# Optimization experiments

Hardware: AMD Instinct MI355X
Metric: run time of the kernel (lower is better)

## Reference

```python
import jax, jax.numpy as jnp
import numpy as np

N = 20000      # nodes (spots)
D = 256        # embed_dim
H = 4          # n_heads
DH = D // H    # head dim
L = 2          # n_layers
E = 320000     # edges (avg degree 16)
K = 48         # static padded-neighbor cap (>= true max degree for this data)
EPS = 1e-5
NEG = -1e30


def setup_inputs() -> dict:
    key = jax.random.key(0)
    ks = jax.random.split(key, 8)
    s = 0.05
    return {
        "expr_embed": jax.random.normal(ks[0], (N, D), jnp.float32),
        "spatial_embed": jax.random.normal(ks[1], (N, D), jnp.float32),
        "in_proj_w": jax.random.normal(ks[2], (L, 3 * D, D), jnp.float32) * s,
        "in_proj_b": jnp.zeros((L, 3 * D), jnp.float32),
        "out_proj_w": jax.random.normal(ks[3], (L, D, D), jnp.float32) * s,
        "out_proj_b": jnp.zeros((L, D), jnp.float32),
        "ffn_w1": jax.random.normal(ks[4], (L, 2 * D, D), jnp.float32) * s,
        "ffn_b1": jnp.zeros((L, 2 * D), jnp.float32),
        "ffn_w2": jax.random.normal(ks[5], (L, D, 2 * D), jnp.float32) * s,
        "ffn_b2": jnp.zeros((L, D), jnp.float32),
        "ln1_g": jnp.ones((L, D), jnp.float32),
        "ln1_b": jnp.zeros((L, D), jnp.float32),
        "ln2_g": jnp.ones((L, D), jnp.float32),
        "ln2_b": jnp.zeros((L, D), jnp.float32),
        "edge_index": jax.random.randint(ks[6], (2, E), 0, N, jnp.int32),
    }


def _build_neighbors(edge_index):
    """Padded neighbor indices (N,K) and key_padding_mask (N,K) (True = pad)."""
    src, tgt = edge_index[0], edge_index[1]
    counts = jnp.zeros((N,), jnp.int32).at[tgt].add(1)
    order = jnp.argsort(tgt)                       # group edges by target
    src_s, tgt_s = src[order], tgt[order]
    offsets = jnp.concatenate([jnp.zeros((1,), jnp.int32),
                               jnp.cumsum(counts)[:-1].astype(jnp.int32)])
    pos = jnp.arange(E, dtype=jnp.int32) - offsets[tgt_s]
    pos = jnp.where(pos < K, pos, K)               # K is out-of-bounds -> dropped
    nbr = jnp.zeros((N, K), jnp.int32).at[tgt_s, pos].set(src_s, mode='drop')
    pad = jnp.ones((N, K), bool).at[tgt_s, pos].set(False, mode='drop')
    iso = counts == 0                              # isolated spots attend to self
    nbr = nbr.at[:, 0].set(jnp.where(iso, jnp.arange(N, dtype=jnp.int32), nbr[:, 0]))
    pad = pad.at[:, 0].set(jnp.where(iso, False, pad[:, 0]))
    return nbr, pad


def _layernorm(x, g, b):
    mu = jnp.mean(x, -1, keepdims=True)
    var = jnp.var(x, -1, keepdims=True)
    return (x - mu) * jax.lax.rsqrt(var + EPS) * g + b


def _forward(expr_embed, spatial_embed, in_proj_w, in_proj_b, out_proj_w,
             out_proj_b, ffn_w1, ffn_b1, ffn_w2, ffn_b2,
             ln1_g, ln1_b, ln2_g, ln2_b, nbr, pad):
    x = expr_embed
    scale = 1.0 / jnp.sqrt(jnp.asarray(DH, x.dtype))
    for i in range(L):
        Wq, Wk, Wv = jnp.split(in_proj_w[i], 3, axis=0)
        bq, bk, bv = jnp.split(in_proj_b[i], 3, axis=0)
        q = (x @ Wq.T + bq).reshape(N, H, DH)
        # project spatial once, gather projected rows (same math as gather-then-project)
        k = (spatial_embed @ Wk.T + bk)[nbr].reshape(N, K, H, DH)
        v = (spatial_embed @ Wv.T + bv)[nbr].reshape(N, K, H, DH)
        scores = jnp.einsum('nhd,nkhd->nhk', q, k) * scale      # (N,H,K)
        scores = jnp.where(pad[:, None, :], NEG, scores)
        attn = jax.nn.softmax(scores, axis=-1)
        ao = jnp.einsum('nhk,nkhd->nhd', attn, v).reshape(N, D)
        ao = ao @ out_proj_w[i].T + out_proj_b[i]
        x = _layernorm(x + ao, ln1_g[i], ln1_b[i])
        h = jax.nn.gelu(x @ ffn_w1[i].T + ffn_b1[i], approximate=False)
        h = h @ ffn_w2[i].T + ffn_b2[i]
        x = _layernorm(x + h, ln2_g[i], ln2_b[i])
    return x


def reference(expr_embed, spatial_embed, in_proj_w, in_proj_b, out_proj_w,
              out_proj_b, ffn_w1, ffn_b1, ffn_w2, ffn_b2,
              ln1_g, ln1_b, ln2_g, ln2_b, edge_index):
    nbr, pad = _build_neighbors(edge_index.astype(jnp.int32))
    return _forward(expr_embed, spatial_embed, in_proj_w, in_proj_b, out_proj_w,
                    out_proj_b, ffn_w1, ffn_b1, ffn_w2, ffn_b2,
                    ln1_g, ln1_b, ln2_g, ln2_b, nbr, pad)
```

## Files before the change

kernel.cpp:

```cpp
#include <hip/hip_runtime.h>

#define N_NODES 20000
#define DIM 256
#define NHEAD 4
#define DHEAD 64
#define NLAYER 2
#define NEDGE 320000
#define KCAP 48
#define NBM64 313
#define NBM32 625

typedef __bf16 v8bf __attribute__((ext_vector_type(8)));
typedef __bf16 v2bf __attribute__((ext_vector_type(2)));
typedef float v4f __attribute__((ext_vector_type(4)));

union U32 { unsigned u; v2bf v; };

__device__ __forceinline__ unsigned short f2bf(float f) {
    unsigned u = __float_as_uint(f);
    unsigned r = u + 0x7FFFu + ((u >> 16) & 1u);
    return (unsigned short)(r >> 16);
}
__device__ __forceinline__ float bflo(unsigned u) { return __uint_as_float(u << 16); }
__device__ __forceinline__ float bfhi(unsigned u) { return __uint_as_float(u & 0xFFFF0000u); }

__device__ __forceinline__ void gl2lds(const void* g, void* l) {
    __builtin_amdgcn_global_load_lds(
        (const __attribute__((address_space(1))) unsigned int*)g,
        (__attribute__((address_space(3))) unsigned int*)l, 16, 0, 0);
}

__device__ __forceinline__ void stage8(const unsigned short* __restrict__ g0,
                                       size_t stride_e, unsigned short* lds) {
    const int l = threadIdx.x & 63;
    const int r = l >> 3;
    const int c = (l & 7) ^ r;
    gl2lds(g0 + (size_t)r * stride_e + c * 8, lds);
}
__device__ __forceinline__ void stage8c(const unsigned short* __restrict__ base,
                                        int row0, int rowmax, size_t stride_e,
                                        int k0, unsigned short* lds) {
    const int l = threadIdx.x & 63;
    const int r = l >> 3;
    const int c = (l & 7) ^ r;
    int row = row0 + r; row = row > rowmax ? rowmax : row;
    gl2lds(base + (size_t)row * stride_e + k0 + c * 8, lds);
}

__device__ __forceinline__ v8bf frag_read(const unsigned short* lds, int row, int col2) {
    const int bo = row * 128 + (col2 ^ ((row & 7) << 4));
    return *(const v8bf*)((const char*)lds + bo);
}

__global__ void sniffzero_kernel(const unsigned short* __restrict__ p,
                                 int* __restrict__ flag, int* __restrict__ cnt) {
    if (blockIdx.x == 0) {
        __shared__ int s;
        if (threadIdx.x == 0) s = 0;
        __syncthreads();
        int c = 0;
        for (int i = threadIdx.x; i < 4096; i += 256) {
            unsigned short u = p[i];
            unsigned e = (u >> 7) & 0xFFu;
            if (e == 0xFFu) c++;
            else if (e == 0u && (u & 0x7Fu)) c++;
        }
        atomicAdd(&s, c);
        __syncthreads();
        if (threadIdx.x == 0) flag[0] = (s >= 4) ? 1 : 0;
    } else {
        int i = (blockIdx.x - 1) * 256 + threadIdx.x;
        if (i < N_NODES) cnt[i] = 0;
    }
}

struct ConvBfArgs { const void* src[6]; unsigned short* dst[6]; int n[6]; };
struct ConvF32Args { const void* src[8]; float* dst[8]; int n[8]; };

__global__ void prep_kernel(ConvBfArgs a, ConvF32Args cf,
                            const int* __restrict__ ei,
                            int* __restrict__ cnt, int* __restrict__ nbr,
                            const int* __restrict__ flag) {
    const int y = blockIdx.y;
    if (y < 6) {
        const int n  = a.n[y];
        const int i0 = (blockIdx.x * 256 + threadIdx.x) * 4;
        if (i0 >= n) return;
        unsigned short* dst = a.dst[y];
        if (flag[0]) {
            float4 v = *(const float4*)((const float*)a.src[y] + i0);
            ushort4 o;
            o.x = f2bf(v.x); o.y = f2bf(v.y); o.z = f2bf(v.z); o.w = f2bf(v.w);
            *(ushort4*)(dst + i0) = o;
        } else {
            ushort4 u = *(const ushort4*)((const unsigned short*)a.src[y] + i0);
            *(ushort4*)(dst + i0) = u;
        }
    } else if (y == 6) {
        if (blockIdx.x >= 2) return;
        const int i0 = (blockIdx.x * 256 + threadIdx.x) * 4;
        const int f = flag[0];
#pragma unroll
        for (int t = 0; t < 8; ++t) {
            const int n = cf.n[t];
            if (i0 >= n) continue;
            float* dst = cf.dst[t];
            if (f) {
                float4 v = *(const float4*)((const float*)cf.src[t] + i0);
                *(float4*)(dst + i0) = v;
            } else {
                ushort4 u = *(const ushort4*)((const unsigned short*)cf.src[t] + i0);
                *(float4*)(dst + i0) =
                    make_float4(bflo(u.x), bflo(u.y), bflo(u.z), bflo(u.w));
            }
        }
    } else {
        const int e = blockIdx.x * 256 + threadIdx.x;
        if (e >= NEDGE) return;
        int s = ei[e];
        int t = ei[NEDGE + e];
        int slot = atomicAdd(&cnt[t], 1);
        if (slot < KCAP) nbr[t * KCAP + slot] = s;
    }
}

__device__ __forceinline__ void gemm_body64(
    unsigned short* At, unsigned short* Bt,
    const unsigned short* __restrict__ A, const unsigned short* __restrict__ B,
    const float* __restrict__ bias, unsigned short* __restrict__ C,
    int M, int Nc, int Kd, int m0, int nB, int nC, int do_gelu)
{
    const int tid  = threadIdx.x;
    const int wave = tid >> 6;
    const int lane = tid & 63;
    const int wr   = (wave >> 1) * 32;
    const int wc   = (wave & 1) * 64;
    const int lm   = lane & 15;
    const int lk   = (lane >> 4) * 8;

    v4f acc[2][4] = {};

    for (int k0 = 0; k0 < Kd; k0 += 64) {
#pragma unroll
        for (int i = 0; i < 2; ++i) {
            const int rr = wave * 16 + i * 8;
            stage8c(A, m0 + rr, M - 1, Kd, k0, At + rr * 64);
        }
#pragma unroll
        for (int i = 0; i < 4; ++i) {
            const int rr = wave * 32 + i * 8;
            stage8(B + (size_t)(nB + rr) * Kd + k0, Kd, Bt + rr * 64);
        }
        __syncthreads();

#pragma unroll
        for (int ks = 0; ks < 2; ++ks) {
            v8bf af[2], bq[4];
#pragma unroll
            for (int mi = 0; mi < 2; ++mi)
                af[mi] = frag_read(At, wr + mi * 16 + lm, (ks * 32 + lk) * 2);
#pragma unroll
            for (int ni = 0; ni < 4; ++ni)
                bq[ni] = frag_read(Bt, wc + ni * 16 + lm, (ks * 32 + lk) * 2);
#pragma unroll
            for (int mi = 0; mi < 2; ++mi)
#pragma unroll
                for (int ni = 0; ni < 4; ++ni)
                    acc[mi][ni] = __builtin_amdgcn_mfma_f32_16x16x32_bf16(
                        af[mi], bq[ni], acc[mi][ni], 0, 0, 0);
        }
        __syncthreads();
    }

    const int rq = (lane >> 4) << 2;
#pragma unroll
    for (int ni = 0; ni < 4; ++ni) {
        int colb = wc + ni * 16 + lm;
        float bv = bias[nB + colb];
        int colc = nC + colb;
#pragma unroll
        for (int mi = 0; mi < 2; ++mi) {
#pragma unroll
            for (int r = 0; r < 4; ++r) {
                int row = m0 + wr + mi * 16 + rq + r;
                if (row >= M) continue;
                float v = acc[mi][ni][r] + bv;
                if (do_gelu) v = 0.5f * v * (1.0f + erff(v * 0.7071067811865475f));
                C[(size_t)row * Nc + colc] = f2bf(v);
            }
        }
    }
}

__global__ __launch_bounds__(256) void gemm_kernel(
    const unsigned short* __restrict__ A, const unsigned short* __restrict__ B,
    const float* __restrict__ bias, unsigned short* __restrict__ C,
    int M, int Nc, int Kd, int do_gelu)
{
    __shared__ __align__(1024) unsigned short At[64 * 64];
    __shared__ __align__(1024) unsigned short Bt[128 * 64];
    const int n0 = blockIdx.y * 128;
    gemm_body64(At, Bt, A, B, bias, C, M, Nc, Kd, blockIdx.x * 64, n0, n0, do_gelu);
}

__global__ __launch_bounds__(256) void qkv_kernel(
    const unsigned short* __restrict__ x, const unsigned short* __restrict__ spat,
    const unsigned short* __restrict__ W, const float* __restrict__ bias,
    unsigned short* __restrict__ q, unsigned short* __restrict__ kv, int M)
{
    __shared__ __align__(1024) unsigned short At[64 * 64];
    __shared__ __align__(1024) unsigned short Bt[128 * 64];
    const int y = blockIdx.y;
    const unsigned short* A = (y < 2) ? x : spat;
    unsigned short*       C = (y < 2) ? q : kv;
    const int Nc = (y < 2) ? 256 : 512;
    const int nB = y * 128;
    const int nC = (y < 2) ? nB : nB - 256;
    gemm_body64(At, Bt, A, W, bias, C, M, Nc, 256, blockIdx.x * 64, nB, nC, 0);
}

__global__ __launch_bounds__(256) void gemm_ln_kernel(
    const unsigned short* __restrict__ A, const unsigned short* __restrict__ B,
    const float* __restrict__ bias, const unsigned short* __restrict__ xres,
    const float* __restrict__ g, const float* __restrict__ bb,
    unsigned short* __restrict__ xout, void* __restrict__ dout,
    int M, int Kd, int final_out, const int* __restrict__ flag)
{
    __shared__ __align__(1024) unsigned short At[32 * 64];
    __shared__ __align__(1024) unsigned short Bt[256 * 64];
    __shared__ float partS[4][32], partSS[4][32];
    __shared__ float totMu[32], totR[32];

    const int tid  = threadIdx.x;
    const int m0   = blockIdx.x * 32;
    const int wave = tid >> 6;
    const int lane = tid & 63;
    const int wn0  = wave * 64;
    const int lm   = lane & 15;
    const int lk   = (lane >> 4) * 8;

    v4f acc[2][4] = {};

    for (int k0 = 0; k0 < Kd; k0 += 64) {
        {
            const int rr = wave * 8;
            stage8c(A, m0 + rr, M - 1, Kd, k0, At + rr * 64);
        }
#pragma unroll
        for (int i = 0; i < 8; ++i) {
            const int rr = wave * 64 + i * 8;
            stage8(B + (size_t)rr * Kd + k0, Kd, Bt + rr * 64);
        }
        __syncthreads();

#pragma unroll
        for (int ks = 0; ks < 2; ++ks) {
            v8bf af[2], bq[4];
#pragma unroll
            for (int mi = 0; mi < 2; ++mi)
                af[mi] = frag_read(At, mi * 16 + lm, (ks * 32 + lk) * 2);
#pragma unroll
            for (int ni = 0; ni < 4; ++ni)
                bq[ni] = frag_read(Bt, wn0 + ni * 16 + lm, (ks * 32 + lk) * 2);
#pragma unroll
            for (int mi = 0; mi < 2; ++mi)
#pragma unroll
                for (int ni = 0; ni < 4; ++ni)
                    acc[mi][ni] = __builtin_amdgcn_mfma_f32_16x16x32_bf16(
                        af[mi], bq[ni], acc[mi][ni], 0, 0, 0);
        }
        __syncthreads();
    }

    const int rq = (lane >> 4) << 2;
    float gv[4], bv2[4], biasv[4];
#pragma unroll
    for (int ni = 0; ni < 4; ++ni) {
        int col = wn0 + ni * 16 + lm;
        biasv[ni] = bias[col];
        gv[ni]    = g[col];
        bv2[ni]   = bb[col];
    }

    float sl[2][4] = {}, ssl[2][4] = {};
#pragma unroll
    for (int mi = 0; mi < 2; ++mi) {
#pragma unroll
        for (int r = 0; r < 4; ++r) {
            int row = m0 + mi * 16 + rq + r;
#pragma unroll
            for (int ni = 0; ni < 4; ++ni) {
                int col = wn0 + ni * 16 + lm;
                float resv = bflo((unsigned)xres[(size_t)row * DIM + col]);
                float v = acc[mi][ni][r] + biasv[ni] + resv;
                acc[mi][ni][r] = v;
                sl[mi][r]  += v;
                ssl[mi][r] += v * v;
            }
        }
    }
#pragma unroll
    for (int mi = 0; mi < 2; ++mi)
#pragma unroll
        for (int r = 0; r < 4; ++r) {
#pragma unroll
            for (int m = 1; m <= 8; m <<= 1) {
                sl[mi][r]  += __shfl_xor(sl[mi][r],  m, 64);
                ssl[mi][r] += __shfl_xor(ssl[mi][r], m, 64);
            }
        }
    if (lm == 0) {
#pragma unroll
        for (int mi = 0; mi < 2; ++mi)
#pragma unroll
            for (int r = 0; r < 4; ++r) {
                partS[wave][mi * 16 + rq + r]  = sl[mi][r];
                partSS[wave][mi * 16 + rq + r] = ssl[mi][r];
            }
    }
    __syncthreads();
    if (tid < 32) {
        float S = partS[0][tid] + partS[1][tid] + partS[2][tid] + partS[3][tid];
        float SS = partSS[0][tid] + partSS[1][tid] + partSS[2][tid] + partSS[3][tid];
        float mu  = S * (1.0f / DIM);
        float var = SS * (1.0f / DIM) - mu * mu;
        totMu[tid] = mu;
        totR[tid]  = rsqrtf(var + 1e-5f);
    }
    __syncthreads();

#pragma unroll
    for (int mi = 0; mi < 2; ++mi) {
#pragma unroll
        for (int r = 0; r < 4; ++r) {
            int lrow = mi * 16 + rq + r;
            int row  = m0 + lrow;
            float mu = totMu[lrow];
            float rv = totR[lrow];
#pragma unroll
            for (int ni = 0; ni < 4; ++ni) {
                int col = wn0 + ni * 16 + lm;
                float o = (acc[mi][ni][r] - mu) * rv * gv[ni] + bv2[ni];
                if (final_out) {
                    if (flag[0]) ((float*)dout)[(size_t)row * DIM + col] = o;
                    else ((unsigned short*)dout)[(size_t)row * DIM + col] = f2bf(o);
                } else {
                    xout[(size_t)row * DIM + col] = f2bf(o);
                }
            }
        }
    }
}

__global__ __launch_bounds__(256) void attn_kernel(
    const unsigned short* __restrict__ q,
    const unsigned short* __restrict__ kv,
    const int* __restrict__ nbr,
    const int* __restrict__ cnt,
    unsigned short* __restrict__ ao)
{
    const int n    = blockIdx.x;
    const int tid  = threadIdx.x;
    const int h    = tid >> 6;
    const int lane = tid & 63;

    __shared__ float sc[NHEAD][KCAP];
    __shared__ int   nbs[NHEAD][KCAP];

    int deg = cnt[n];
    if (deg > KCAP) deg = KCAP;
    const bool iso = (deg == 0);
    if (iso) deg = 1;

    if (lane < KCAP)
        nbs[h][lane] = (lane < deg) ? (iso ? n : nbr[n * KCAP + lane]) : 0;

    const int sub = lane & 7;
    const int grp = lane >> 3;
    const uint4 qu = *(const uint4*)&q[(size_t)n * DIM + h * DHEAD + sub * 8];
    const unsigned short* kbase = kv + h * DHEAD + sub * 8;
    const int nit = (deg + 7) >> 3;

    const int quarter = lane >> 4;
    const int d0      = (lane & 15) * 4;
    const unsigned short* vbase = kv + 256 + h * DHEAD + d0;
    const int dmax = (deg + 3) & ~3;
    const int npv  = dmax >> 2;

    uint4 ku[6];
#pragma unroll
    for (int it = 0; it < 6; ++it) {
        if (it < nit) {
            int nb = nbs[h][it * 8 + grp];
            ku[it] = *(const uint4*)&kbase[(size_t)nb * 512];
        }
    }
    uint2 vu[8];
#pragma unroll
    for (int it = 0; it < 8; ++it) {
        if (it < npv) {
            int nb = nbs[h][it * 4 + quarter];
            vu[it] = *(const uint2*)&vbase[(size_t)nb * 512];
        }
    }

#pragma unroll
    for (int it = 0; it < 6; ++it) {
        if (it < nit) {
            int j = it * 8 + grp;
            uint4 kz = ku[it];
#if __has_builtin(__builtin_amdgcn_fdot2_f32_bf16)
            U32 a0{qu.x}, a1{qu.y}, a2{qu.z}, a3{qu.w};
            U32 b0{kz.x}, b1{kz.y}, b2{kz.z}, b3{kz.w};
            float p = __builtin_amdgcn_fdot2_f32_bf16(a0.v, b0.v, 0.0f, false);
            p = __builtin_amdgcn_fdot2_f32_bf16(a1.v, b1.v, p, false);
            p = __builtin_amdgcn_fdot2_f32_bf16(a2.v, b2.v, p, false);
            p = __builtin_amdgcn_fdot2_f32_bf16(a3.v, b3.v, p, false);
#else
            float p = bflo(qu.x) * bflo(kz.x);
            p = fmaf(bfhi(qu.x), bfhi(kz.x), p);
            p = fmaf(bflo(qu.y), bflo(kz.y), p);
            p = fmaf(bfhi(qu.y), bfhi(kz.y), p);
            p = fmaf(bflo(qu.z), bflo(kz.z), p);
            p = fmaf(bfhi(qu.z), bfhi(kz.z), p);
            p = fmaf(bflo(qu.w), bflo(kz.w), p);
            p = fmaf(bfhi(qu.w), bfhi(kz.w), p);
#endif
            p += __shfl_xor(p, 1, 64);
            p += __shfl_xor(p, 2, 64);
            p += __shfl_xor(p, 4, 64);
            if (sub == 0 && j < deg) sc[h][j] = p * 0.125f;
        }
    }

    {
        float s  = (lane < deg) ? sc[h][lane] : -1e30f;
        float mx = s;
#pragma unroll
        for (int m = 32; m >= 1; m >>= 1) mx = fmaxf(mx, __shfl_xor(mx, m, 64));
        float e   = (lane < deg) ? __expf(s - mx) : 0.0f;
        float sum = e;
#pragma unroll
        for (int m = 32; m >= 1; m >>= 1) sum += __shfl_xor(sum, m, 64);
        float inv = 1.0f / sum;
        if (lane < KCAP) sc[h][lane] = e * inv;
    }

    {
        float a0 = 0.f, a1 = 0.f, a2 = 0.f, a3 = 0.f;
#pragma unroll
        for (int it = 0; it < 8; ++it) {
            if (it < npv) {
                float w = sc[h][it * 4 + quarter];
                uint2 u = vu[it];
                a0 = fmaf(w, bflo(u.x), a0);
                a1 = fmaf(w, bfhi(u.x), a1);
                a2 = fmaf(w, bflo(u.y), a2);
                a3 = fmaf(w, bfhi(u.y), a3);
            }
        }
        for (int j = 32; j < dmax; j += 4) {
            int j0 = j + quarter;
            int nb = nbs[h][j0];
            uint2 u = *(const uint2*)&vbase[(size_t)nb * 512];
            float w = sc[h][j0];
            a0 = fmaf(w, bflo(u.x), a0);
            a1 = fmaf(w, bfhi(u.x), a1);
            a2 = fmaf(w, bflo(u.y), a2);
            a3 = fmaf(w, bfhi(u.y), a3);
        }
        a0 += __shfl_xor(a0, 16, 64); a0 += __shfl_xor(a0, 32, 64);
        a1 += __shfl_xor(a1, 16, 64); a1 += __shfl_xor(a1, 32, 64);
        a2 += __shfl_xor(a2, 16, 64); a2 += __shfl_xor(a2, 32, 64);
        a3 += __shfl_xor(a3, 16, 64); a3 += __shfl_xor(a3, 32, 64);
        if (lane < 16) {
            uint2 o;
            o.x = (unsigned)f2bf(a0) | ((unsigned)f2bf(a1) << 16);
            o.y = (unsigned)f2bf(a2) | ((unsigned)f2bf(a3) << 16);
            *(uint2*)&ao[(size_t)n * DIM + h * DHEAD + d0] = o;
        }
    }
}

extern "C" void kernel_launch(void* const* d_in, const int* in_sizes, int n_in,
                              void* d_out, int out_size, void* d_ws, size_t ws_size,
                              hipStream_t stream) {
    const int* ei = (const int*)d_in[14];

    char* ws = (char*)d_ws;
    size_t off = 0;
    auto alloc = [&](size_t bytes) -> void* {
        void* p = ws + off;
        off = (off + bytes + 255) & ~(size_t)255;
        return p;
    };

    const int bidx[6] = { 0, 1, 2, 4, 6, 8 };
    const int bnn[6]  = { N_NODES * DIM, N_NODES * DIM,
                          NLAYER * 3 * DIM * DIM, NLAYER * DIM * DIM,
                          NLAYER * 2 * DIM * DIM, NLAYER * DIM * 2 * DIM };
    ConvBfArgs cb;
    unsigned short* canb[6];
    for (int i = 0; i < 6; ++i) {
        canb[i] = (unsigned short*)alloc((size_t)bnn[i] * 2);
        cb.src[i] = d_in[bidx[i]];
        cb.dst[i] = canb[i];
        cb.n[i]   = bnn[i];
    }
    const unsigned short* expr_b = canb[0];
    const unsigned short* spat_b = canb[1];
    const unsigned short* ipw    = canb[2];
    const unsigned short* opw    = canb[3];
    const unsigned short* w1     = canb[4];
    const unsigned short* w2     = canb[5];

    const int fidx[8] = { 3, 5, 7, 9, 10, 11, 12, 13 };
    const int fn[8]   = { NLAYER * 3 * DIM, NLAYER * DIM, NLAYER * 2 * DIM,
                          NLAYER * DIM, NLAYER * DIM, NLAYER * DIM,
                          NLAYER * DIM, NLAYER * DIM };
    ConvF32Args cf;
    float* canf[8];
    for (int i = 0; i < 8; ++i) {
        canf[i] = (float*)alloc((size_t)fn[i] * 4);
        cf.src[i] = d_in[fidx[i]];
        cf.dst[i] = canf[i];
        cf.n[i]   = fn[i];
    }

    unsigned short* x_buf  = (unsigned short*)alloc((size_t)N_NODES * DIM * 2);
    unsigned short* q_buf  = (unsigned short*)alloc((size_t)N_NODES * DIM * 2);
    unsigned short* kv_buf = (unsigned short*)alloc((size_t)N_NODES * 2 * DIM * 2);
    unsigned short* ao_buf = (unsigned short*)alloc((size_t)N_NODES * DIM * 2);
    unsigned short* h_buf  = (unsigned short*)alloc((size_t)N_NODES * 2 * DIM * 2);
    int* cnt  = (int*)alloc((size_t)N_NODES * 4);
    int* nbr  = (int*)alloc((size_t)N_NODES * KCAP * 4);
    int* flag = (int*)alloc(256);

    sniffzero_kernel<<<1 + (N_NODES + 255) / 256, 256, 0, stream>>>(
        (const unsigned short*)d_in[0], flag, cnt);
    prep_kernel<<<dim3((N_NODES * DIM) / 1024, 8), 256, 0, stream>>>(
        cb, cf, ei, cnt, nbr, flag);

    for (int i = 0; i < NLAYER; ++i) {
        const unsigned short* Wqkv = ipw + (size_t)i * 3 * DIM * DIM;
        const float*          bqkv = canf[0] + (size_t)i * 3 * DIM;
        const unsigned short* xin  = (i == 0) ? expr_b : x_buf;

        qkv_kernel<<<dim3(NBM64, 6), 256, 0, stream>>>(
            xin, spat_b, Wqkv, bqkv, q_buf, kv_buf, N_NODES);
        attn_kernel<<<N_NODES, 256, 0, stream>>>(q_buf, kv_buf, nbr, cnt, ao_buf);
        gemm_ln_kernel<<<NBM32, 256, 0, stream>>>(
            ao_buf, opw + (size_t)i * DIM * DIM, canf[1] + (size_t)i * DIM,
            xin, canf[4] + (size_t)i * DIM, canf[5] + (size_t)i * DIM,
            x_buf, nullptr, N_NODES, DIM, 0, flag);
        gemm_kernel<<<dim3(NBM64, 4), 256, 0, stream>>>(
            x_buf, w1 + (size_t)i * 2 * DIM * DIM, canf[2] + (size_t)i * 2 * DIM,
            h_buf, N_NODES, 2 * DIM, DIM, 1);
        gemm_ln_kernel<<<NBM32, 256, 0, stream>>>(
            h_buf, w2 + (size_t)i * DIM * 2 * DIM, canf[3] + (size_t)i * DIM,
            x_buf, canf[6] + (size_t)i * DIM, canf[7] + (size_t)i * DIM,
            x_buf, d_out, N_NODES, 2 * DIM, (i == NLAYER - 1) ? 1 : 0, flag);
    }
}
```

Before: 398.3 us.

## Replace LDS-staged GEMM tiles with direct global-to-register double-buffered fragment loads

GEMM and GEMM+LayerNorm kernels stop staging A/B tiles through shared memory with global_load_lds and barriers. Each wave now loads its MFMA fragments directly from global memory into registers, double-buffered two K-tiles ahead, with K as a template constant so the loop fully unrolls. This removes LDS traffic and __syncthreads stalls. In exchange, waves no longer share tile loads, so global/L2 traffic and register pressure rise.

```diff
diff --git a/kernel.cpp b/kernel.cpp
--- a/kernel.cpp
+++ b/kernel.cpp
@@ -23,34 +23,6 @@
 }
 __device__ __forceinline__ float bflo(unsigned u) { return __uint_as_float(u << 16); }
 __device__ __forceinline__ float bfhi(unsigned u) { return __uint_as_float(u & 0xFFFF0000u); }
-
-__device__ __forceinline__ void gl2lds(const void* g, void* l) {
-    __builtin_amdgcn_global_load_lds(
-        (const __attribute__((address_space(1))) unsigned int*)g,
-        (__attribute__((address_space(3))) unsigned int*)l, 16, 0, 0);
-}
-
-__device__ __forceinline__ void stage8(const unsigned short* __restrict__ g0,
-                                       size_t stride_e, unsigned short* lds) {
-    const int l = threadIdx.x & 63;
-    const int r = l >> 3;
-    const int c = (l & 7) ^ r;
-    gl2lds(g0 + (size_t)r * stride_e + c * 8, lds);
-}
-__device__ __forceinline__ void stage8c(const unsigned short* __restrict__ base,
-                                        int row0, int rowmax, size_t stride_e,
-                                        int k0, unsigned short* lds) {
-    const int l = threadIdx.x & 63;
-    const int r = l >> 3;
-    const int c = (l & 7) ^ r;
-    int row = row0 + r; row = row > rowmax ? rowmax : row;
-    gl2lds(base + (size_t)row * stride_e + k0 + c * 8, lds);
-}
-
-__device__ __forceinline__ v8bf frag_read(const unsigned short* lds, int row, int col2) {
-    const int bo = row * 128 + (col2 ^ ((row & 7) << 4));
-    return *(const v8bf*)((const char*)lds + bo);
-}
 
 __global__ void sniffzero_kernel(const unsigned short* __restrict__ p,
                                  int* __restrict__ flag, int* __restrict__ cnt) {
@@ -124,11 +96,11 @@
     }
 }
 
-__device__ __forceinline__ void gemm_body64(
-    unsigned short* At, unsigned short* Bt,
+template<int KD>
+__device__ __forceinline__ void dgemm_tile64(
     const unsigned short* __restrict__ A, const unsigned short* __restrict__ B,
     const float* __restrict__ bias, unsigned short* __restrict__ C,
-    int M, int Nc, int Kd, int m0, int nB, int nC, int do_gelu)
+    int M, int Nc, int m0, int nB, int nC, int do_gelu)
 {
     const int tid  = threadIdx.x;
     const int wave = tid >> 6;
@@ -137,39 +109,45 @@
     const int wc   = (wave & 1) * 64;
     const int lm   = lane & 15;
     const int lk   = (lane >> 4) * 8;
+    constexpr int NT = KD / 64;
+
+    int ar[2];
+    ar[0] = m0 + wr + lm;       if (ar[0] > M - 1) ar[0] = M - 1;
+    ar[1] = m0 + wr + 16 + lm;  if (ar[1] > M - 1) ar[1] = M - 1;
+    const int br0 = nB + wc + lm;
+
+    v8bf af[2][2][2];
+    v8bf bq[2][4][2];
+
+    auto LOADT = [&](int buf, int t) {
+        const int k0 = t * 64 + lk;
+#pragma unroll
+        for (int mi = 0; mi < 2; ++mi)
+#pragma unroll
+            for (int ks = 0; ks < 2; ++ks)
+                af[buf][mi][ks] = *(const v8bf*)&A[(size_t)ar[mi] * KD + k0 + ks * 32];
+#pragma unroll
+        for (int ni = 0; ni < 4; ++ni)
+#pragma unroll
+            for (int ks = 0; ks < 2; ++ks)
+                bq[buf][ni][ks] = *(const v8bf*)&B[(size_t)(br0 + ni * 16) * KD + k0 + ks * 32];
+    };
 
     v4f acc[2][4] = {};
-
-    for (int k0 = 0; k0 < Kd; k0 += 64) {
-#pragma unroll
-        for (int i = 0; i < 2; ++i) {
-            const int rr = wave * 16 + i * 8;
-            stage8c(A, m0 + rr, M - 1, Kd, k0, At + rr * 64);
-        }
-#pragma unroll
-        for (int i = 0; i < 4; ++i) {
-            const int rr = wave * 32 + i * 8;
-            stage8(B + (size_t)(nB + rr) * Kd + k0, Kd, Bt + rr * 64);
-        }
-        __syncthreads();
-
-#pragma unroll
-        for (int ks = 0; ks < 2; ++ks) {
-            v8bf af[2], bq[4];
-#pragma unroll
-            for (int mi = 0; mi < 2; ++mi)
-                af[mi] = frag_read(At, wr + mi * 16 + lm, (ks * 32 + lk) * 2);
-#pragma unroll
-            for (int ni = 0; ni < 4; ++ni)
-                bq[ni] = frag_read(Bt, wc + ni * 16 + lm, (ks * 32 + lk) * 2);
+    LOADT(0, 0);
+    if (NT > 1) LOADT(1, 1);
+#pragma unroll
+    for (int t = 0; t < NT; ++t) {
+        const int buf = t & 1;
+#pragma unroll
+        for (int ks = 0; ks < 2; ++ks)
 #pragma unroll
             for (int mi = 0; mi < 2; ++mi)
 #pragma unroll
                 for (int ni = 0; ni < 4; ++ni)
                     acc[mi][ni] = __builtin_amdgcn_mfma_f32_16x16x32_bf16(
-                        af[mi], bq[ni], acc[mi][ni], 0, 0, 0);
-        }
-        __syncthreads();
+                        af[buf][mi][ks], bq[buf][ni][ks], acc[mi][ni], 0, 0, 0);
+        if (t + 2 < NT) LOADT(buf, t + 2);
     }
 
     const int rq = (lane >> 4) << 2;
@@ -195,12 +173,10 @@
 __global__ __launch_bounds__(256) void gemm_kernel(
     const unsigned short* __restrict__ A, const unsigned short* __restrict__ B,
     const float* __restrict__ bias, unsigned short* __restrict__ C,
-    int M, int Nc, int Kd, int do_gelu)
-{
-    __shared__ __align__(1024) unsigned short At[64 * 64];
-    __shared__ __align__(1024) unsigned short Bt[128 * 64];
+    int M, int Nc, int do_gelu)
+{
     const int n0 = blockIdx.y * 128;
-    gemm_body64(At, Bt, A, B, bias, C, M, Nc, Kd, blockIdx.x * 64, n0, n0, do_gelu);
+    dgemm_tile64<256>(A, B, bias, C, M, Nc, blockIdx.x * 64, n0, n0, do_gelu);
 }
 
 __global__ __launch_bounds__(256) void qkv_kernel(
@@ -208,26 +184,23 @@
     const unsigned short* __restrict__ W, const float* __restrict__ bias,
     unsigned short* __restrict__ q, unsigned short* __restrict__ kv, int M)
 {
-    __shared__ __align__(1024) unsigned short At[64 * 64];
-    __shared__ __align__(1024) unsigned short Bt[128 * 64];
     const int y = blockIdx.y;
     const unsigned short* A = (y < 2) ? x : spat;
     unsigned short*       C = (y < 2) ? q : kv;
     const int Nc = (y < 2) ? 256 : 512;
     const int nB = y * 128;
     const int nC = (y < 2) ? nB : nB - 256;
-    gemm_body64(At, Bt, A, W, bias, C, M, Nc, 256, blockIdx.x * 64, nB, nC, 0);
-}
-
-__global__ __launch_bounds__(256) void gemm_ln_kernel(
+    dgemm_tile64<256>(A, W, bias, C, M, Nc, blockIdx.x * 64, nB, nC, 0);
+}
+
+template<int KD>
+__device__ __forceinline__ void dgemm_ln_body(
     const unsigned short* __restrict__ A, const unsigned short* __restrict__ B,
     const float* __restrict__ bias, const unsigned short* __restrict__ xres,
     const float* __restrict__ g, const float* __restrict__ bb,
     unsigned short* __restrict__ xout, void* __restrict__ dout,
-    int M, int Kd, int final_out, const int* __restrict__ flag)
-{
-    __shared__ __align__(1024) unsigned short At[32 * 64];
-    __shared__ __align__(1024) unsigned short Bt[256 * 64];
+    int M, int final_out, const int* __restrict__ flag)
+{
     __shared__ float partS[4][32], partSS[4][32];
     __shared__ float totMu[32], totR[32];
 
@@ -238,38 +211,43 @@
     const int wn0  = wave * 64;
     const int lm   = lane & 15;
     const int lk   = (lane >> 4) * 8;
+    constexpr int NT = KD / 64;
+
+    const int ar0 = m0 + lm;
+    const int br0 = wn0 + lm;
+
+    v8bf af[2][2][2];
+    v8bf bq[2][4][2];
+
+    auto LOADT = [&](int buf, int t) {
+        const int k0 = t * 64 + lk;
+#pragma unroll
+        for (int mi = 0; mi < 2; ++mi)
+#pragma unroll
+            for (int ks = 0; ks < 2; ++ks)
+                af[buf][mi][ks] = *(const v8bf*)&A[(size_t)(ar0 + mi * 16) * KD + k0 + ks * 32];
+#pragma unroll
+        for (int ni = 0; ni < 4; ++ni)
+#pragma unroll
+            for (int ks = 0; ks < 2; ++ks)
+                bq[buf][ni][ks] = *(const v8bf*)&B[(size_t)(br0 + ni * 16) * KD + k0 + ks * 32];
+    };
 
     v4f acc[2][4] = {};
-
-    for (int k0 = 0; k0 < Kd; k0 += 64) {
-        {
-            const int rr = wave * 8;
-            stage8c(A, m0 + rr, M - 1, Kd, k0, At + rr * 64);
-        }
-#pragma unroll
-        for (int i = 0; i < 8; ++i) {
-            const int rr = wave * 64 + i * 8;
-            stage8(B + (size_t)rr * Kd + k0, Kd, Bt + rr * 64);
-        }
-        __syncthreads();
-
-#pragma unroll
-        for (int ks = 0; ks < 2; ++ks) {
-            v8bf af[2], bq[4];
-#pragma unroll
-            for (int mi = 0; mi < 2; ++mi)
-                af[mi] = frag_read(At, mi * 16 + lm, (ks * 32 + lk) * 2);
-#pragma unroll
-            for (int ni = 0; ni < 4; ++ni)
-                bq[ni] = frag_read(Bt, wn0 + ni * 16 + lm, (ks * 32 + lk) * 2);
+    LOADT(0, 0);
+    if (NT > 1) LOADT(1, 1);
+#pragma unroll
+    for (int t = 0; t < NT; ++t) {
+        const int buf = t & 1;
+#pragma unroll
+        for (int ks = 0; ks < 2; ++ks)
 #pragma unroll
             for (int mi = 0; mi < 2; ++mi)
 #pragma unroll
                 for (int ni = 0; ni < 4; ++ni)
                     acc[mi][ni] = __builtin_amdgcn_mfma_f32_16x16x32_bf16(
-                        af[mi], bq[ni], acc[mi][ni], 0, 0, 0);
-        }
-        __syncthreads();
+                        af[buf][mi][ks], bq[buf][ni][ks], acc[mi][ni], 0, 0, 0);
+        if (t + 2 < NT) LOADT(buf, t + 2);
     }
 
     const int rq = (lane >> 4) << 2;
@@ -350,6 +328,26 @@
             }
         }
     }
+}
+
+__global__ __launch_bounds__(256) void gemm_ln256_kernel(
+    const unsigned short* __restrict__ A, const unsigned short* __restrict__ B,
+    const float* __restrict__ bias, const unsigned short* __restrict__ xres,
+    const float* __restrict__ g, const float* __restrict__ bb,
+    unsigned short* __restrict__ xout, void* __restrict__ dout,
+    int M, int final_out, const int* __restrict__ flag)
+{
+    dgemm_ln_body<256>(A, B, bias, xres, g, bb, xout, dout, M, final_out, flag);
+}
+
+__global__ __launch_bounds__(256) void gemm_ln512_kernel(
+    const unsigned short* __restrict__ A, const unsigned short* __restrict__ B,
+    const float* __restrict__ bias, const unsigned short* __restrict__ xres,
+    const float* __restrict__ g, const float* __restrict__ bb,
+    unsigned short* __restrict__ xout, void* __restrict__ dout,
+    int M, int final_out, const int* __restrict__ flag)
+{
+    dgemm_ln_body<512>(A, B, bias, xres, g, bb, xout, dout, M, final_out, flag);
 }
 
 __global__ __launch_bounds__(256) void attn_kernel(
@@ -549,16 +547,16 @@
         qkv_kernel<<<dim3(NBM64, 6), 256, 0, stream>>>(
             xin, spat_b, Wqkv, bqkv, q_buf, kv_buf, N_NODES);
         attn_kernel<<<N_NODES, 256, 0, stream>>>(q_buf, kv_buf, nbr, cnt, ao_buf);
-        gemm_ln_kernel<<<NBM32, 256, 0, stream>>>(
+        gemm_ln256_kernel<<<NBM32, 256, 0, stream>>>(
             ao_buf, opw + (size_t)i * DIM * DIM, canf[1] + (size_t)i * DIM,
             xin, canf[4] + (size_t)i * DIM, canf[5] + (size_t)i * DIM,
-            x_buf, nullptr, N_NODES, DIM, 0, flag);
+            x_buf, nullptr, N_NODES, 0, flag);
         gemm_kernel<<<dim3(NBM64, 4), 256, 0, stream>>>(
             x_buf, w1 + (size_t)i * 2 * DIM * DIM, canf[2] + (size_t)i * 2 * DIM,
-            h_buf, N_NODES, 2 * DIM, DIM, 1);
-        gemm_ln_kernel<<<NBM32, 256, 0, stream>>>(
+            h_buf, N_NODES, 2 * DIM, 1);
+        gemm_ln512_kernel<<<NBM32, 256, 0, stream>>>(
             h_buf, w2 + (size_t)i * DIM * 2 * DIM, canf[3] + (size_t)i * DIM,
             x_buf, canf[6] + (size_t)i * DIM, canf[7] + (size_t)i * DIM,
-            x_buf, d_out, N_NODES, 2 * DIM, (i == NLAYER - 1) ? 1 : 0, flag);
-    }
-}
+            x_buf, d_out, N_NODES, (i == NLAYER - 1) ? 1 : 0, flag);
+    }
+}
```

Measured after the change: 538.7 us. 1.35x slower.
